# Kernel optimization log

Measured on AMD Instinct MI355X. Metric: run time of the kernel, lower is better.

Reference implementation:

```python
import jax, jax.numpy as jnp
import numpy as np

E = 256  # embed_dim (hardcoded in source module)
H = 4    # n_head
D = E // H
SEQ = 32768


def setup_inputs() -> dict:
    key = jax.random.key(0)
    ks = jax.random.split(key, 5)
    x = jax.random.normal(ks[0], (SEQ, E), dtype=jnp.float32)
    in_proj_weight = jax.random.normal(ks[1], (3 * E, E), dtype=jnp.float32) * (1.0 / np.sqrt(E))
    in_proj_bias = jax.random.normal(ks[2], (3 * E,), dtype=jnp.float32) * 0.02
    out_proj_weight = jax.random.normal(ks[3], (E, E), dtype=jnp.float32) * (1.0 / np.sqrt(E))
    out_proj_bias = jax.random.normal(ks[4], (E,), dtype=jnp.float32) * 0.02
    return {
        "x": x,
        "in_proj_weight": in_proj_weight,
        "in_proj_bias": in_proj_bias,
        "out_proj_weight": out_proj_weight,
        "out_proj_bias": out_proj_bias,
    }


def reference(x, in_proj_weight, in_proj_bias, out_proj_weight, out_proj_bias):
    # QKV projections (q uses only the first token of x: single-query decode attention)
    Wq, Wk, Wv = in_proj_weight[:E], in_proj_weight[E:2 * E], in_proj_weight[2 * E:]
    bq, bk, bv = in_proj_bias[:E], in_proj_bias[E:2 * E], in_proj_bias[2 * E:]
    q = x[:1] @ Wq.T + bq            # [1, E]
    k = x @ Wk.T + bk                # [S, E]
    v = x @ Wv.T + bv                # [S, E]

    qh = q.reshape(H, D)             # [H, D] (single query)
    kh = k.reshape(-1, H, D)         # [S, H, D]
    vh = v.reshape(-1, H, D)         # [S, H, D]

    scale = 1.0 / np.sqrt(D).astype(np.float32)
    scores = jnp.einsum("hd,shd->hs", qh, kh) * scale   # [H, S]
    attn = jax.nn.softmax(scores, axis=-1)                # [H, S]
    ctx = jnp.einsum("hs,shd->hd", attn, vh)             # [H, D]

    out = ctx.reshape(1, E) @ out_proj_weight.T + out_proj_bias  # [1, E]
    return out
```

## Files before the change

### kernel.cpp

```cpp
#include <hip/hip_runtime.h>

#define S 32768
#define NBLK 256
#define WS_C4   0
#define WS_KQ   64
#define WS_MP   1088
#define WS_LP   2112
#define WS_YV   3136
#define WS_B2   4160
#define WS_M2   4416
#define WS_YP   266560
#define WS_CNT  528704

__device__ __forceinline__ float dot4(float4 a, float4 b) {
  return a.x * b.x + a.y * b.y + a.z * b.z + a.w * b.w;
}

__device__ __forceinline__ void signal_done(int* p) {
  __threadfence();
  __syncthreads();
  if (threadIdx.x == 0) atomicAdd(p, 1);
}
__device__ __forceinline__ void spin_until(int* p, int target) {
  if (threadIdx.x == 0) {
    while (atomicAdd(p, 0) < target) __builtin_amdgcn_s_sleep(2);
  }
  __syncthreads();
  __threadfence();
}
__device__ __forceinline__ int take_ticket(int* p, int* shi) {
  __threadfence();
  __syncthreads();
  if (threadIdx.x == 0) *shi = atomicAdd(p, 1);
  __syncthreads();
  return *shi;
}

__device__ __forceinline__ void phaseA_kq(const float* __restrict__ x, const float* __restrict__ W,
                                          const float* __restrict__ inb, float* __restrict__ kq,
                                          float* __restrict__ c4, float* sh, int bid, int t) {
  float* xs = sh;
  float* qls = sh + 256;
  float* red = sh + 320;
  const int lane = t & 63, w = t >> 6;
  const int h = bid >> 2, qt = bid & 3;
  if (t < 256) xs[t] = x[t];
  __syncthreads();
  const float4 xv = *(const float4*)&xs[lane * 4];
#pragma unroll
  for (int k = 0; k < 8; ++k) {
    const int eloc = w * 8 + k;
    const int row = h * 64 + eloc;
    float4 wv = *(const float4*)&W[(size_t)row * 256 + lane * 4];
    float p = dot4(wv, xv);
#pragma unroll
    for (int m = 1; m < 64; m <<= 1) p += __shfl_xor(p, m);
    if (lane == 0) qls[eloc] = p + inb[row];
  }
  __syncthreads();
  const int cl = t & 63, ds = t >> 6;
  float acc = 0.f;
#pragma unroll
  for (int d2 = 0; d2 < 8; ++d2) {
    const int d = ds * 8 + d2;
    acc += W[(size_t)(256 + h * 64 + d) * 256 + qt * 64 + cl] * qls[d];
  }
  red[ds * 64 + cl] = acc;
  __syncthreads();
  if (ds == 0) {
    float s = 0.f;
#pragma unroll
    for (int i = 0; i < 8; ++i) s += red[i * 64 + cl];
    kq[h * 256 + qt * 64 + cl] = s;
  }
  if (qt == 0 && t < 64) {
    float v = qls[t] * inb[256 + h * 64 + t];
#pragma unroll
    for (int m = 1; m < 64; m <<= 1) v += __shfl_xor(v, m);
    if (t == 0) c4[h] = v;
  }
}

__device__ __forceinline__ void phaseA_m2(const float* __restrict__ W, const float* __restrict__ Wout,
                                          float* __restrict__ M2, float* sh, int b2, int t) {
  float* wout_t = sh;
  const int tile = b2 >> 1, sub = b2 & 1;
  const int h = tile >> 4, e0 = (tile & 15) * 16 + sub * 8;
  {
    const int e = t >> 6, d = t & 63;
    wout_t[e * 64 + d] = Wout[(size_t)(e0 + e) * 256 + h * 64 + d];
  }
  __syncthreads();
  const int c = t & 255, eh = t >> 8;
  float acc[4] = {0.f, 0.f, 0.f, 0.f};
#pragma unroll 8
  for (int d = 0; d < 64; ++d) {
    const float wv = W[(size_t)(512 + h * 64 + d) * 256 + c];
#pragma unroll
    for (int e = 0; e < 4; ++e) acc[e] += wv * wout_t[(eh * 4 + e) * 64 + d];
  }
#pragma unroll
  for (int e = 0; e < 4; ++e)
    M2[(size_t)(e0 + eh * 4 + e) * 1024 + h * 256 + c] = acc[e];
}

__device__ __forceinline__ void phaseA_b2(const float* __restrict__ Wout, const float* __restrict__ inb,
                                          const float* __restrict__ bout, float* __restrict__ bias2,
                                          float* sh, int b, int t) {
  float* red = sh;
  const int og = t >> 5, seg = t & 31;
  const int e = b * 16 + og;
  float acc = 0.f;
#pragma unroll
  for (int j = 0; j < 8; ++j)
    acc += Wout[(size_t)e * 256 + seg * 8 + j] * inb[512 + seg * 8 + j];
  red[og * 32 + seg] = acc;
  __syncthreads();
  if (t < 16) {
    float s = bout[b * 16 + t];
#pragma unroll
    for (int i = 0; i < 32; ++i) s += red[t * 32 + i];
    bias2[b * 16 + t] = s;
  }
}

__device__ __forceinline__ float bscore(float4 xv, float4 kq0, float4 kq1, float4 kq2,
                                        float4 kq3, float c4v, int lane) {
  float p0 = dot4(xv, kq0), p1 = dot4(xv, kq1), p2 = dot4(xv, kq2), p3 = dot4(xv, kq3);
  const bool b1 = (lane & 2) != 0;
  float keep0 = b1 ? p2 : p0, send0 = b1 ? p0 : p2;
  keep0 += __shfl_xor(send0, 2);
  float keep1 = b1 ? p3 : p1, send1 = b1 ? p1 : p3;
  keep1 += __shfl_xor(send1, 2);
  const bool b0 = (lane & 1) != 0;
  float vv = b0 ? keep1 : keep0, sv = b0 ? keep0 : keep1;
  vv += __shfl_xor(sv, 1);
  vv += __shfl_xor(vv, 4);
  vv += __shfl_xor(vv, 8);
  vv += __shfl_xor(vv, 16);
  vv += __shfl_xor(vv, 32);
  return (vv + c4v) * 0.125f;
}

__device__ __forceinline__ void phaseB_core(const float4* xvA, const float4* xvB,
                                            const float* __restrict__ kq, const float* __restrict__ c4,
                                            float* __restrict__ ypart, float* __restrict__ mpart,
                                            float* __restrict__ lpart, float* sh, int bid, int t) {
  float* yls = sh;
  float* sml = sh + 8192;
  float* sll = sh + 8224;
  const int lane = t & 63, w = t >> 6;
  const int hme = lane & 3;
  const float4 kq0 = *(const float4*)&kq[0 * 256 + lane * 4];
  const float4 kq1 = *(const float4*)&kq[1 * 256 + lane * 4];
  const float4 kq2 = *(const float4*)&kq[2 * 256 + lane * 4];
  const float4 kq3 = *(const float4*)&kq[3 * 256 + lane * 4];
  const float c4v = c4[hme];

  float vA[8];
#pragma unroll
  for (int r = 0; r < 8; ++r) vA[r] = bscore(xvA[r], kq0, kq1, kq2, kq3, c4v, lane);
  float m = vA[0];
#pragma unroll
  for (int r = 1; r < 8; ++r) m = fmaxf(m, vA[r]);

  float l = 0.f;
  float4 a[4];
#pragma unroll
  for (int k = 0; k < 4; ++k) a[k] = (float4){0.f, 0.f, 0.f, 0.f};
#pragma unroll
  for (int r = 0; r < 8; ++r) {
    const float e0 = __expf(vA[r] - m);
    l += e0;
    const float e1 = __shfl_xor(e0, 1);
    const float e2 = __shfl_xor(e0, 2);
    const float e3 = __shfl_xor(e0, 3);
    a[0].x += e0 * xvA[r].x; a[0].y += e0 * xvA[r].y; a[0].z += e0 * xvA[r].z; a[0].w += e0 * xvA[r].w;
    a[1].x += e1 * xvA[r].x; a[1].y += e1 * xvA[r].y; a[1].z += e1 * xvA[r].z; a[1].w += e1 * xvA[r].w;
    a[2].x += e2 * xvA[r].x; a[2].y += e2 * xvA[r].y; a[2].z += e2 * xvA[r].z; a[2].w += e2 * xvA[r].w;
    a[3].x += e3 * xvA[r].x; a[3].y += e3 * xvA[r].y; a[3].z += e3 * xvA[r].z; a[3].w += e3 * xvA[r].w;
  }

  float vB[8];
#pragma unroll
  for (int r = 0; r < 8; ++r) vB[r] = bscore(xvB[r], kq0, kq1, kq2, kq3, c4v, lane);
  float mB = vB[0];
#pragma unroll
  for (int r = 1; r < 8; ++r) mB = fmaxf(mB, vB[r]);

  {
    const float mN = fmaxf(m, mB);
    const float fown = __expf(m - mN);
    l *= fown;
    const float f1 = __shfl_xor(fown, 1);
    const float f2 = __shfl_xor(fown, 2);
    const float f3 = __shfl_xor(fown, 3);
    a[0].x *= fown; a[0].y *= fown; a[0].z *= fown; a[0].w *= fown;
    a[1].x *= f1;   a[1].y *= f1;   a[1].z *= f1;   a[1].w *= f1;
    a[2].x *= f2;   a[2].y *= f2;   a[2].z *= f2;   a[2].w *= f2;
    a[3].x *= f3;   a[3].y *= f3;   a[3].z *= f3;   a[3].w *= f3;
    m = mN;
  }
#pragma unroll
  for (int r = 0; r < 8; ++r) {
    const float e0 = __expf(vB[r] - m);
    l += e0;
    const float e1 = __shfl_xor(e0, 1);
    const float e2 = __shfl_xor(e0, 2);
    const float e3 = __shfl_xor(e0, 3);
    a[0].x += e0 * xvB[r].x; a[0].y += e0 * xvB[r].y; a[0].z += e0 * xvB[r].z; a[0].w += e0 * xvB[r].w;
    a[1].x += e1 * xvB[r].x; a[1].y += e1 * xvB[r].y; a[1].z += e1 * xvB[r].z; a[1].w += e1 * xvB[r].w;
    a[2].x += e2 * xvB[r].x; a[2].y += e2 * xvB[r].y; a[2].z += e2 * xvB[r].z; a[2].w += e2 * xvB[r].w;
    a[3].x += e3 * xvB[r].x; a[3].y += e3 * xvB[r].y; a[3].z += e3 * xvB[r].z; a[3].w += e3 * xvB[r].w;
  }

  __syncthreads();
  if (lane < 4) { sml[w * 4 + lane] = m; sll[w * 4 + lane] = l; }
  __syncthreads();

#pragma unroll
  for (int k = 0; k < 4; ++k) {
    const int h = hme ^ k;
    float mb = sml[h];
#pragma unroll
    for (int i = 1; i < 8; ++i) mb = fmaxf(mb, sml[i * 4 + h]);
    const float f = __expf(sml[w * 4 + h] - mb);
    float4 av;
    av.x = a[k].x * f; av.y = a[k].y * f; av.z = a[k].z * f; av.w = a[k].w * f;
    *(float4*)&yls[w * 1024 + h * 256 + lane * 4] = av;
  }
  __syncthreads();

  if (t < 4) {
    float mb = sml[t];
#pragma unroll
    for (int i = 1; i < 8; ++i) mb = fmaxf(mb, sml[i * 4 + t]);
    float lb = 0.f;
#pragma unroll
    for (int i = 0; i < 8; ++i) lb += sll[i * 4 + t] * __expf(sml[i * 4 + t] - mb);
    mpart[t * NBLK + bid] = mb;
    lpart[t * NBLK + bid] = lb;
  }
  float* yp = &ypart[(size_t)bid * 1024];
#pragma unroll
  for (int o = t; o < 1024; o += 512) {
    float s = 0.f;
#pragma unroll
    for (int i = 0; i < 8; ++i) s += yls[i * 1024 + o];
    yp[o] = s;
  }
}

__device__ __forceinline__ void phaseC(const float* __restrict__ ypart, const float* __restrict__ mpart,
                                       const float* __restrict__ lpart, float* __restrict__ yv,
                                       float* sh, int bid, int t) {
  float* mred = sh;
  float* scales = sh + 256;
  float* lred = sh + 512;
  float* sred = sh + 768;
  const int h = bid >> 4;
  const int o0 = bid * 16;
  if (t < 256) mred[t] = mpart[h * 256 + t];
  __syncthreads();
  for (int s = 128; s > 0; s >>= 1) {
    if (t < s) mred[t] = fmaxf(mred[t], mred[t + s]);
    __syncthreads();
  }
  const float mg = mred[0];
  if (t < 256) {
    const float sc = __expf(mpart[h * 256 + t] - mg);
    scales[t] = sc;
    lred[t] = lpart[h * 256 + t] * sc;
  }
  __syncthreads();
  for (int s = 128; s > 0; s >>= 1) {
    if (t < s) lred[t] += lred[t + s];
    __syncthreads();
  }
  const float inv = 1.0f / lred[0];
  const int ol = t & 15, bg = t >> 4;
  float s = 0.f;
#pragma unroll
  for (int j = 0; j < 8; ++j) {
    const int b = bg * 8 + j;
    s += ypart[(size_t)b * 1024 + o0 + ol] * scales[b];
  }
  sred[bg * 16 + ol] = s;
  __syncthreads();
  if (t < 16) {
    float tot = 0.f;
#pragma unroll
    for (int g = 0; g < 32; ++g) tot += sred[g * 16 + t];
    yv[o0 + t] = tot * inv;
  }
}

__device__ __forceinline__ void phaseD(const float* __restrict__ M2, const float* __restrict__ yv,
                                       const float* __restrict__ bias2, float* __restrict__ out,
                                       float* sh, int bid, int t) {
  float* yls = sh;
  float* smo = sh + 1024;
  for (int i = t; i < 1024; i += 512) yls[i] = yv[i];
  __syncthreads();
  const int og = t >> 5, seg = t & 31;
  const int e = bid * 16 + og;
  float acc = 0.f;
  const float4* m4 = (const float4*)&M2[(size_t)e * 1024 + seg * 32];
  const float4* y4 = (const float4*)&yls[seg * 32];
#pragma unroll
  for (int j = 0; j < 8; ++j) acc += dot4(m4[j], y4[j]);
  smo[og * 32 + seg] = acc;
  __syncthreads();
  if (t < 16) {
    float s = bias2[bid * 16 + t];
#pragma unroll
    for (int i = 0; i < 32; ++i) s += smo[t * 32 + i];
    out[bid * 16 + t] = s;
  }
}

__global__ void __launch_bounds__(512, 1) mha_coop(const float* __restrict__ x,
                                                   const float* __restrict__ W,
                                                   const float* __restrict__ inb,
                                                   const float* __restrict__ Wout,
                                                   const float* __restrict__ bout,
                                                   float* __restrict__ out,
                                                   float* __restrict__ ws) {
  __shared__ __align__(16) float sh[8448];
  __shared__ int shi;
  const int t = threadIdx.x, bid = blockIdx.x;
  const int lane = t & 63, w = t >> 6;
  int* cnt = (int*)(ws + WS_CNT);
  float* c4 = ws + WS_C4;
  float* kq = ws + WS_KQ;
  float* mpart = ws + WS_MP;
  float* lpart = ws + WS_LP;
  float* yv = ws + WS_YV;
  float* bias2 = ws + WS_B2;
  float* M2 = ws + WS_M2;
  float* ypart = ws + WS_YP;

  const int r0 = bid * 128 + w * 16;
  float4 xvA[8], xvB[8];

  if (bid >= 16) {
#pragma unroll
    for (int r = 0; r < 8; ++r)
      xvA[r] = *(const float4*)&x[(size_t)(r0 + r) * 256 + lane * 4];
#pragma unroll
    for (int r = 0; r < 8; ++r)
      xvB[r] = *(const float4*)&x[(size_t)(r0 + 8 + r) * 256 + lane * 4];
  }

  if (bid < 16) {
    phaseA_kq(x, W, inb, kq, c4, sh, bid, t);
    signal_done(&cnt[0]);
#pragma unroll
    for (int r = 0; r < 8; ++r)
      xvA[r] = *(const float4*)&x[(size_t)(r0 + r) * 256 + lane * 4];
#pragma unroll
    for (int r = 0; r < 8; ++r)
      xvB[r] = *(const float4*)&x[(size_t)(r0 + 8 + r) * 256 + lane * 4];
  } else if (bid < 144) {
    phaseA_m2(W, Wout, M2, sh, bid - 16, t);
    signal_done(&cnt[1]);
  } else if (bid < 160) {
    phaseA_b2(Wout, inb, bout, bias2, sh, bid - 144, t);
    signal_done(&cnt[1]);
  }

  spin_until(&cnt[0], 16);
  phaseB_core(xvA, xvB, kq, c4, ypart, mpart, lpart, sh, bid, t);

  const int tk = take_ticket(&cnt[2], &shi);
  if (tk < NBLK - 64) return;
  spin_until(&cnt[2], NBLK);
  phaseC(ypart, mpart, lpart, yv, sh, tk - (NBLK - 64), t);

  const int t2 = take_ticket(&cnt[3], &shi);
  if (t2 < 48) return;
  spin_until(&cnt[3], 64);
  spin_until(&cnt[1], 144);
  phaseD(M2, yv, bias2, out, sh, t2 - 48, t);
}

__global__ void __launch_bounds__(512) fb_A(const float* __restrict__ x, const float* __restrict__ W,
                                            const float* __restrict__ inb, const float* __restrict__ Wout,
                                            const float* __restrict__ bout, float* __restrict__ ws) {
  __shared__ __align__(16) float sh[832];
  const int bid = blockIdx.x, t = threadIdx.x;
  if (bid < 16) phaseA_kq(x, W, inb, ws + WS_KQ, ws + WS_C4, sh, bid, t);
  else if (bid < 144) phaseA_m2(W, Wout, ws + WS_M2, sh, bid - 16, t);
  else if (bid < 160) phaseA_b2(Wout, inb, bout, ws + WS_B2, sh, bid - 144, t);
}
__global__ void __launch_bounds__(512) fb_B(const float* __restrict__ x, float* __restrict__ ws) {
  __shared__ __align__(16) float sh[8256];
  const int bid = blockIdx.x, t = threadIdx.x;
  const int lane = t & 63, w = t >> 6;
  const int r0 = bid * 128 + w * 16;
  float4 xvA[8], xvB[8];
#pragma unroll
  for (int r = 0; r < 8; ++r)
    xvA[r] = *(const float4*)&x[(size_t)(r0 + r) * 256 + lane * 4];
#pragma unroll
  for (int r = 0; r < 8; ++r)
    xvB[r] = *(const float4*)&x[(size_t)(r0 + 8 + r) * 256 + lane * 4];
  phaseB_core(xvA, xvB, ws + WS_KQ, ws + WS_C4, ws + WS_YP, ws + WS_MP, ws + WS_LP, sh, bid, t);
}
__global__ void __launch_bounds__(512) fb_C(float* __restrict__ ws) {
  __shared__ __align__(16) float sh[1280];
  phaseC(ws + WS_YP, ws + WS_MP, ws + WS_LP, ws + WS_YV, sh, blockIdx.x, threadIdx.x);
}
__global__ void __launch_bounds__(512) fb_D(float* __restrict__ out, float* __restrict__ ws) {
  __shared__ __align__(16) float sh[1536];
  phaseD(ws + WS_M2, ws + WS_YV, ws + WS_B2, out, sh, blockIdx.x, threadIdx.x);
}

extern "C" void kernel_launch(void* const* d_in, const int* in_sizes, int n_in,
                              void* d_out, int out_size, void* d_ws, size_t ws_size,
                              hipStream_t stream) {
  const float* x = (const float*)d_in[0];
  const float* W = (const float*)d_in[1];
  const float* inb = (const float*)d_in[2];
  const float* Wout = (const float*)d_in[3];
  const float* bout = (const float*)d_in[4];
  float* out = (float*)d_out;
  float* ws = (float*)d_ws;

  hipMemsetAsync((void*)(ws + WS_CNT), 0, 16, stream);

  int dev = 0;
  (void)hipGetDevice(&dev);
  int coopAttr = 0, ncu = 0, occ = 0;
  bool coop = (hipDeviceGetAttribute(&coopAttr, hipDeviceAttributeCooperativeLaunch, dev) == hipSuccess) &&
              coopAttr != 0;
  coop = coop &&
         (hipDeviceGetAttribute(&ncu, hipDeviceAttributeMultiprocessorCount, dev) == hipSuccess);
  coop = coop &&
         (hipOccupancyMaxActiveBlocksPerMultiprocessor(&occ, mha_coop, 512, 0) == hipSuccess);
  coop = coop && (occ * ncu >= NBLK);

  if (coop) {
    void* args[] = {(void*)&x, (void*)&W, (void*)&inb, (void*)&Wout,
                    (void*)&bout, (void*)&out, (void*)&ws};
    if (hipLaunchCooperativeKernel((const void*)mha_coop, dim3(NBLK), dim3(512),
                                   args, 0, stream) == hipSuccess)
      return;
  }
  fb_A<<<160, 512, 0, stream>>>(x, W, inb, Wout, bout, ws);
  fb_B<<<NBLK, 512, 0, stream>>>(x, ws);
  fb_C<<<64, 512, 0, stream>>>(ws);
  fb_D<<<16, 512, 0, stream>>>(out, ws);
}
```

Before: 36.03 us.

## Compute kq redundantly per block and replace ticket spins with grid sync

Every block now computes the full Wk^T q vector and per-head bias constants in shared memory, so the start of the score phase no longer waits on a global counter. The M2 and bias2 precomputation moves to run after the score phase in the upper blocks. Inter-phase coordination uses a cooperative-groups grid.sync followed by a single acquire counter before the final projection, which is split across 64 blocks instead of 16. This trades redundant weight reads in every block for fewer global synchronization points and a shorter critical path.

```diff
diff --git a/kernel.cpp b/kernel.cpp
--- a/kernel.cpp
+++ b/kernel.cpp
@@ -1,84 +1,88 @@
 #include <hip/hip_runtime.h>
-
-#define S 32768
+#include <hip/hip_cooperative_groups.h>
+namespace cg = cooperative_groups;
+
 #define NBLK 256
-#define WS_C4   0
-#define WS_KQ   64
-#define WS_MP   1088
-#define WS_LP   2112
-#define WS_YV   3136
-#define WS_B2   4160
-#define WS_M2   4416
-#define WS_YP   266560
-#define WS_CNT  528704
+#define WS_MP   0
+#define WS_LP   1024
+#define WS_YV   2048
+#define WS_B2   3072
+#define WS_M2   3328
+#define WS_YP   265472
+#define WS_CNT  527616
 
 __device__ __forceinline__ float dot4(float4 a, float4 b) {
   return a.x * b.x + a.y * b.y + a.z * b.z + a.w * b.w;
 }
 
-__device__ __forceinline__ void signal_done(int* p) {
+__device__ __forceinline__ void sig_rel(int* p) {
   __threadfence();
   __syncthreads();
   if (threadIdx.x == 0) atomicAdd(p, 1);
 }
-__device__ __forceinline__ void spin_until(int* p, int target) {
+__device__ __forceinline__ void spin_acq(int* p, int target) {
   if (threadIdx.x == 0) {
-    while (atomicAdd(p, 0) < target) __builtin_amdgcn_s_sleep(2);
+    while (__hip_atomic_load(p, __ATOMIC_ACQUIRE, __HIP_MEMORY_SCOPE_AGENT) < target)
+      __builtin_amdgcn_s_sleep(8);
   }
   __syncthreads();
   __threadfence();
 }
-__device__ __forceinline__ int take_ticket(int* p, int* shi) {
-  __threadfence();
-  __syncthreads();
-  if (threadIdx.x == 0) *shi = atomicAdd(p, 1);
-  __syncthreads();
-  return *shi;
-}
-
-__device__ __forceinline__ void phaseA_kq(const float* __restrict__ x, const float* __restrict__ W,
-                                          const float* __restrict__ inb, float* __restrict__ kq,
-                                          float* __restrict__ c4, float* sh, int bid, int t) {
-  float* xs = sh;
-  float* qls = sh + 256;
-  float* red = sh + 320;
+
+__device__ __forceinline__ void make_kq(const float* __restrict__ x, const float* __restrict__ W,
+                                        const float* __restrict__ inb,
+                                        float* xs, float* qls, float* kqls, float* c4ls,
+                                        float* red2, int t) {
   const int lane = t & 63, w = t >> 6;
-  const int h = bid >> 2, qt = bid & 3;
   if (t < 256) xs[t] = x[t];
   __syncthreads();
-  const float4 xv = *(const float4*)&xs[lane * 4];
-#pragma unroll
-  for (int k = 0; k < 8; ++k) {
-    const int eloc = w * 8 + k;
-    const int row = h * 64 + eloc;
-    float4 wv = *(const float4*)&W[(size_t)row * 256 + lane * 4];
-    float p = dot4(wv, xv);
-#pragma unroll
-    for (int m = 1; m < 64; m <<= 1) p += __shfl_xor(p, m);
-    if (lane == 0) qls[eloc] = p + inb[row];
-  }
-  __syncthreads();
-  const int cl = t & 63, ds = t >> 6;
-  float acc = 0.f;
-#pragma unroll
-  for (int d2 = 0; d2 < 8; ++d2) {
-    const int d = ds * 8 + d2;
-    acc += W[(size_t)(256 + h * 64 + d) * 256 + qt * 64 + cl] * qls[d];
-  }
-  red[ds * 64 + cl] = acc;
-  __syncthreads();
-  if (ds == 0) {
-    float s = 0.f;
-#pragma unroll
-    for (int i = 0; i < 8; ++i) s += red[i * 64 + cl];
-    kq[h * 256 + qt * 64 + cl] = s;
-  }
-  if (qt == 0 && t < 64) {
-    float v = qls[t] * inb[256 + h * 64 + t];
+  const float4 xv0 = *(const float4*)&xs[lane * 4];
+  for (int k = 0; k < 32; k += 4) {
+    float p[4];
+#pragma unroll
+    for (int j = 0; j < 4; ++j) {
+      const int row = w * 32 + k + j;
+      float4 wv = *(const float4*)&W[(size_t)row * 256 + lane * 4];
+      p[j] = dot4(wv, xv0);
+    }
+#pragma unroll
+    for (int m = 1; m < 64; m <<= 1) {
+#pragma unroll
+      for (int j = 0; j < 4; ++j) p[j] += __shfl_xor(p[j], m);
+    }
+    if (lane == 0) {
+#pragma unroll
+      for (int j = 0; j < 4; ++j) qls[w * 32 + k + j] = p[j] + inb[w * 32 + k + j];
+    }
+  }
+  __syncthreads();
+  const int c = t & 255, g = t >> 8;
+  float acc0 = 0.f, acc1 = 0.f, acc2 = 0.f, acc3 = 0.f;
+#pragma unroll 4
+  for (int dd = 0; dd < 32; ++dd) {
+    const int d = g * 32 + dd;
+    acc0 += W[(size_t)(256 + 0 * 64 + d) * 256 + c] * qls[0 * 64 + d];
+    acc1 += W[(size_t)(256 + 1 * 64 + d) * 256 + c] * qls[1 * 64 + d];
+    acc2 += W[(size_t)(256 + 2 * 64 + d) * 256 + c] * qls[2 * 64 + d];
+    acc3 += W[(size_t)(256 + 3 * 64 + d) * 256 + c] * qls[3 * 64 + d];
+  }
+  red2[g * 1024 + 0 * 256 + c] = acc0;
+  red2[g * 1024 + 1 * 256 + c] = acc1;
+  red2[g * 1024 + 2 * 256 + c] = acc2;
+  red2[g * 1024 + 3 * 256 + c] = acc3;
+  __syncthreads();
+  if (g == 0) {
+#pragma unroll
+    for (int h = 0; h < 4; ++h)
+      kqls[h * 256 + c] = red2[h * 256 + c] + red2[1024 + h * 256 + c];
+  } else {
+    const int hh = w - 4;
+    float v = qls[hh * 64 + lane] * inb[256 + hh * 64 + lane];
 #pragma unroll
     for (int m = 1; m < 64; m <<= 1) v += __shfl_xor(v, m);
-    if (t == 0) c4[h] = v;
-  }
+    if (lane == 0) c4ls[hh] = v;
+  }
+  __syncthreads();
 }
 
 __device__ __forceinline__ void phaseA_m2(const float* __restrict__ W, const float* __restrict__ Wout,
@@ -143,12 +147,11 @@
 }
 
 __device__ __forceinline__ void phaseB_core(const float4* xvA, const float4* xvB,
-                                            const float* __restrict__ kq, const float* __restrict__ c4,
+                                            const float* kq, const float* c4,
                                             float* __restrict__ ypart, float* __restrict__ mpart,
-                                            float* __restrict__ lpart, float* sh, int bid, int t) {
-  float* yls = sh;
-  float* sml = sh + 8192;
-  float* sll = sh + 8224;
+                                            float* __restrict__ lpart, float* yls, int bid, int t) {
+  float* sml = yls + 8192;
+  float* sll = yls + 8224;
   const int lane = t & 63, w = t >> 6;
   const int hme = lane & 3;
   const float4 kq0 = *(const float4*)&kq[0 * 256 + lane * 4];
@@ -295,107 +298,42 @@
   }
 }
 
-__device__ __forceinline__ void phaseD(const float* __restrict__ M2, const float* __restrict__ yv,
-                                       const float* __restrict__ bias2, float* __restrict__ out,
-                                       float* sh, int bid, int t) {
-  float* yls = sh;
+__device__ __forceinline__ void phaseD4(const float* __restrict__ M2, const float* __restrict__ yv,
+                                        const float* __restrict__ bias2, float* __restrict__ out,
+                                        float* sh, int bid, int t) {
+  float* yls2 = sh;
   float* smo = sh + 1024;
-  for (int i = t; i < 1024; i += 512) yls[i] = yv[i];
-  __syncthreads();
-  const int og = t >> 5, seg = t & 31;
-  const int e = bid * 16 + og;
-  float acc = 0.f;
-  const float4* m4 = (const float4*)&M2[(size_t)e * 1024 + seg * 32];
-  const float4* y4 = (const float4*)&yls[seg * 32];
-#pragma unroll
-  for (int j = 0; j < 8; ++j) acc += dot4(m4[j], y4[j]);
-  smo[og * 32 + seg] = acc;
-  __syncthreads();
-  if (t < 16) {
-    float s = bias2[bid * 16 + t];
-#pragma unroll
-    for (int i = 0; i < 32; ++i) s += smo[t * 32 + i];
-    out[bid * 16 + t] = s;
-  }
-}
-
-__global__ void __launch_bounds__(512, 1) mha_coop(const float* __restrict__ x,
-                                                   const float* __restrict__ W,
-                                                   const float* __restrict__ inb,
-                                                   const float* __restrict__ Wout,
-                                                   const float* __restrict__ bout,
-                                                   float* __restrict__ out,
-                                                   float* __restrict__ ws) {
-  __shared__ __align__(16) float sh[8448];
-  __shared__ int shi;
-  const int t = threadIdx.x, bid = blockIdx.x;
   const int lane = t & 63, w = t >> 6;
-  int* cnt = (int*)(ws + WS_CNT);
-  float* c4 = ws + WS_C4;
-  float* kq = ws + WS_KQ;
-  float* mpart = ws + WS_MP;
-  float* lpart = ws + WS_LP;
-  float* yv = ws + WS_YV;
+  for (int i = t; i < 1024; i += 512) yls2[i] = yv[i];
+  __syncthreads();
+  const int eidx = t >> 7, seg = t & 127;
+  const int e = bid * 4 + eidx;
+  const float4* m4 = (const float4*)&M2[(size_t)e * 1024];
+  const float4* y4 = (const float4*)yls2;
+  float acc = dot4(m4[seg * 2], y4[seg * 2]) + dot4(m4[seg * 2 + 1], y4[seg * 2 + 1]);
+#pragma unroll
+  for (int m = 1; m < 64; m <<= 1) acc += __shfl_xor(acc, m);
+  if (lane == 0) smo[w] = acc;
+  __syncthreads();
+  if (t < 4) out[bid * 4 + t] = smo[2 * t] + smo[2 * t + 1] + bias2[bid * 4 + t];
+}
+
+__device__ __forceinline__ void phase1(const float* __restrict__ x, const float* __restrict__ W,
+                                       const float* __restrict__ inb, const float* __restrict__ Wout,
+                                       const float* __restrict__ bout, float* sh, float* ws,
+                                       int bid, int t) {
   float* bias2 = ws + WS_B2;
   float* M2 = ws + WS_M2;
   float* ypart = ws + WS_YP;
-
-  const int r0 = bid * 128 + w * 16;
-  float4 xvA[8], xvB[8];
-
-  if (bid >= 16) {
-#pragma unroll
-    for (int r = 0; r < 8; ++r)
-      xvA[r] = *(const float4*)&x[(size_t)(r0 + r) * 256 + lane * 4];
-#pragma unroll
-    for (int r = 0; r < 8; ++r)
-      xvB[r] = *(const float4*)&x[(size_t)(r0 + 8 + r) * 256 + lane * 4];
-  }
-
-  if (bid < 16) {
-    phaseA_kq(x, W, inb, kq, c4, sh, bid, t);
-    signal_done(&cnt[0]);
-#pragma unroll
-    for (int r = 0; r < 8; ++r)
-      xvA[r] = *(const float4*)&x[(size_t)(r0 + r) * 256 + lane * 4];
-#pragma unroll
-    for (int r = 0; r < 8; ++r)
-      xvB[r] = *(const float4*)&x[(size_t)(r0 + 8 + r) * 256 + lane * 4];
-  } else if (bid < 144) {
-    phaseA_m2(W, Wout, M2, sh, bid - 16, t);
-    signal_done(&cnt[1]);
-  } else if (bid < 160) {
-    phaseA_b2(Wout, inb, bout, bias2, sh, bid - 144, t);
-    signal_done(&cnt[1]);
-  }
-
-  spin_until(&cnt[0], 16);
-  phaseB_core(xvA, xvB, kq, c4, ypart, mpart, lpart, sh, bid, t);
-
-  const int tk = take_ticket(&cnt[2], &shi);
-  if (tk < NBLK - 64) return;
-  spin_until(&cnt[2], NBLK);
-  phaseC(ypart, mpart, lpart, yv, sh, tk - (NBLK - 64), t);
-
-  const int t2 = take_ticket(&cnt[3], &shi);
-  if (t2 < 48) return;
-  spin_until(&cnt[3], 64);
-  spin_until(&cnt[1], 144);
-  phaseD(M2, yv, bias2, out, sh, t2 - 48, t);
-}
-
-__global__ void __launch_bounds__(512) fb_A(const float* __restrict__ x, const float* __restrict__ W,
-                                            const float* __restrict__ inb, const float* __restrict__ Wout,
-                                            const float* __restrict__ bout, float* __restrict__ ws) {
-  __shared__ __align__(16) float sh[832];
-  const int bid = blockIdx.x, t = threadIdx.x;
-  if (bid < 16) phaseA_kq(x, W, inb, ws + WS_KQ, ws + WS_C4, sh, bid, t);
-  else if (bid < 144) phaseA_m2(W, Wout, ws + WS_M2, sh, bid - 16, t);
-  else if (bid < 160) phaseA_b2(Wout, inb, bout, ws + WS_B2, sh, bid - 144, t);
-}
-__global__ void __launch_bounds__(512) fb_B(const float* __restrict__ x, float* __restrict__ ws) {
-  __shared__ __align__(16) float sh[8256];
-  const int bid = blockIdx.x, t = threadIdx.x;
+  float* mpart = ws + WS_MP;
+  float* lpart = ws + WS_LP;
+  float* xs = sh;
+  float* qls = sh + 256;
+  float* kqls = sh + 512;
+  float* c4ls = sh + 1536;
+  float* red2 = sh + 1540;
+  float* yls = sh + 1540;
+
   const int lane = t & 63, w = t >> 6;
   const int r0 = bid * 128 + w * 16;
   float4 xvA[8], xvB[8];
@@ -405,15 +343,52 @@
 #pragma unroll
   for (int r = 0; r < 8; ++r)
     xvB[r] = *(const float4*)&x[(size_t)(r0 + 8 + r) * 256 + lane * 4];
-  phaseB_core(xvA, xvB, ws + WS_KQ, ws + WS_C4, ws + WS_YP, ws + WS_MP, ws + WS_LP, sh, bid, t);
-}
-__global__ void __launch_bounds__(512) fb_C(float* __restrict__ ws) {
+
+  make_kq(x, W, inb, xs, qls, kqls, c4ls, red2, t);
+  phaseB_core(xvA, xvB, kqls, c4ls, ypart, mpart, lpart, yls, bid, t);
+
+  if (bid >= 128) {
+    phaseA_m2(W, Wout, M2, sh, bid - 128, t);
+    if (bid >= 240) {
+      __syncthreads();
+      phaseA_b2(Wout, inb, bout, bias2, sh, bid - 240, t);
+    }
+  }
+}
+
+__global__ void __launch_bounds__(512, 1) mha_one(const float* __restrict__ x,
+                                                  const float* __restrict__ W,
+                                                  const float* __restrict__ inb,
+                                                  const float* __restrict__ Wout,
+                                                  const float* __restrict__ bout,
+                                                  float* __restrict__ out,
+                                                  float* __restrict__ ws) {
+  __shared__ __align__(16) float sh[9796];
+  const int t = threadIdx.x, bid = blockIdx.x;
+  cg::grid_group grid = cg::this_grid();
+
+  phase1(x, W, inb, Wout, bout, sh, ws, bid, t);
+  grid.sync();
+  if (bid >= 64) return;
+  phaseC(ws + WS_YP, ws + WS_MP, ws + WS_LP, ws + WS_YV, sh, bid, t);
+  sig_rel((int*)(ws + WS_CNT));
+  spin_acq((int*)(ws + WS_CNT), 64);
+  phaseD4(ws + WS_M2, ws + WS_YV, ws + WS_B2, out, sh, bid, t);
+}
+
+__global__ void __launch_bounds__(512) fb_1(const float* __restrict__ x, const float* __restrict__ W,
+                                            const float* __restrict__ inb, const float* __restrict__ Wout,
+                                            const float* __restrict__ bout, float* __restrict__ ws) {
+  __shared__ __align__(16) float sh[9796];
+  phase1(x, W, inb, Wout, bout, sh, ws, blockIdx.x, threadIdx.x);
+}
+__global__ void __launch_bounds__(512) fb_2(float* __restrict__ ws) {
   __shared__ __align__(16) float sh[1280];
   phaseC(ws + WS_YP, ws + WS_MP, ws + WS_LP, ws + WS_YV, sh, blockIdx.x, threadIdx.x);
 }
-__global__ void __launch_bounds__(512) fb_D(float* __restrict__ out, float* __restrict__ ws) {
-  __shared__ __align__(16) float sh[1536];
-  phaseD(ws + WS_M2, ws + WS_YV, ws + WS_B2, out, sh, blockIdx.x, threadIdx.x);
+__global__ void __launch_bounds__(512) fb_3(float* __restrict__ out, float* __restrict__ ws) {
+  __shared__ __align__(16) float sh[1056];
+  phaseD4(ws + WS_M2, ws + WS_YV, ws + WS_B2, out, sh, blockIdx.x, threadIdx.x);
 }
 
 extern "C" void kernel_launch(void* const* d_in, const int* in_sizes, int n_in,
@@ -437,18 +412,17 @@
   coop = coop &&
          (hipDeviceGetAttribute(&ncu, hipDeviceAttributeMultiprocessorCount, dev) == hipSuccess);
   coop = coop &&
-         (hipOccupancyMaxActiveBlocksPerMultiprocessor(&occ, mha_coop, 512, 0) == hipSuccess);
+         (hipOccupancyMaxActiveBlocksPerMultiprocessor(&occ, mha_one, 512, 0) == hipSuccess);
   coop = coop && (occ * ncu >= NBLK);
 
   if (coop) {
     void* args[] = {(void*)&x, (void*)&W, (void*)&inb, (void*)&Wout,
                     (void*)&bout, (void*)&out, (void*)&ws};
-    if (hipLaunchCooperativeKernel((const void*)mha_coop, dim3(NBLK), dim3(512),
+    if (hipLaunchCooperativeKernel((const void*)mha_one, dim3(NBLK), dim3(512),
                                    args, 0, stream) == hipSuccess)
       return;
   }
-  fb_A<<<160, 512, 0, stream>>>(x, W, inb, Wout, bout, ws);
-  fb_B<<<NBLK, 512, 0, stream>>>(x, ws);
-  fb_C<<<64, 512, 0, stream>>>(ws);
-  fb_D<<<16, 512, 0, stream>>>(out, ws);
-}
+  fb_1<<<NBLK, 512, 0, stream>>>(x, W, inb, Wout, bout, ws);
+  fb_2<<<64, 512, 0, stream>>>(ws);
+  fb_3<<<64, 512, 0, stream>>>(out, ws);
+}
```

Result: slower. 54.58 us (+51.5%).

## Replace counter barriers with per-block flags and move M2 work after scores

Applied to the files above, without the earlier changes.

Swaps the shared atomic counters and ticket scheme for per-block release/acquire flags that whole blocks poll with syncthreads_and. The M2/bias2 precomputation moves off the critical path: instead of running before phase B on blocks 16-159, it runs after phase B on blocks 128-255, so phase B can start sooner. Phase D is spread over 64 blocks with wave-shuffle reductions, and the flag memset grows to 2 KB. The cost is more polling traffic, and M2 may now finish late and stall phase D.

```diff
diff --git a/kernel.cpp b/kernel.cpp
--- a/kernel.cpp
+++ b/kernel.cpp
@@ -1,13 +1,12 @@
 #include <hip/hip_runtime.h>
 
-#define S 32768
 #define NBLK 256
-#define WS_C4   0
-#define WS_KQ   64
-#define WS_MP   1088
-#define WS_LP   2112
-#define WS_YV   3136
-#define WS_B2   4160
+#define WS_MP   0
+#define WS_LP   1024
+#define WS_YV   2048
+#define WS_B2   3072
+#define WS_KQ   3328
+#define WS_C4   4352
 #define WS_M2   4416
 #define WS_YP   266560
 #define WS_CNT  528704
@@ -16,24 +15,19 @@
   return a.x * b.x + a.y * b.y + a.z * b.z + a.w * b.w;
 }
 
-__device__ __forceinline__ void signal_done(int* p) {
+__device__ __forceinline__ void set_flag(int* slot, int t) {
   __threadfence();
   __syncthreads();
-  if (threadIdx.x == 0) atomicAdd(p, 1);
-}
-__device__ __forceinline__ void spin_until(int* p, int target) {
-  if (threadIdx.x == 0) {
-    while (atomicAdd(p, 0) < target) __builtin_amdgcn_s_sleep(2);
-  }
-  __syncthreads();
+  if (t == 0) __hip_atomic_store(slot, 1, __ATOMIC_RELEASE, __HIP_MEMORY_SCOPE_AGENT);
+}
+__device__ __forceinline__ void poll_flags(const int* flags, int n, int t) {
+  const int idx = t & (n - 1);
+  for (;;) {
+    int v = __hip_atomic_load((int*)&flags[idx], __ATOMIC_RELAXED, __HIP_MEMORY_SCOPE_AGENT);
+    if (__syncthreads_and(v != 0)) break;
+    __builtin_amdgcn_s_sleep(2);
+  }
   __threadfence();
-}
-__device__ __forceinline__ int take_ticket(int* p, int* shi) {
-  __threadfence();
-  __syncthreads();
-  if (threadIdx.x == 0) *shi = atomicAdd(p, 1);
-  __syncthreads();
-  return *shi;
 }
 
 __device__ __forceinline__ void phaseA_kq(const float* __restrict__ x, const float* __restrict__ W,
@@ -81,8 +75,10 @@
   }
 }
 
-__device__ __forceinline__ void phaseA_m2(const float* __restrict__ W, const float* __restrict__ Wout,
-                                          float* __restrict__ M2, float* sh, int b2, int t) {
+__device__ __forceinline__ void phaseM2b(const float* __restrict__ W, const float* __restrict__ Wout,
+                                         const float* __restrict__ inb, const float* __restrict__ bout,
+                                         float* __restrict__ M2, float* __restrict__ bias2,
+                                         float* sh, int b2, int t) {
   float* wout_t = sh;
   const int tile = b2 >> 1, sub = b2 & 1;
   const int h = tile >> 4, e0 = (tile & 15) * 16 + sub * 8;
@@ -102,26 +98,17 @@
 #pragma unroll
   for (int e = 0; e < 4; ++e)
     M2[(size_t)(e0 + eh * 4 + e) * 1024 + h * 256 + c] = acc[e];
-}
-
-__device__ __forceinline__ void phaseA_b2(const float* __restrict__ Wout, const float* __restrict__ inb,
-                                          const float* __restrict__ bout, float* __restrict__ bias2,
-                                          float* sh, int b, int t) {
+  __syncthreads();
   float* red = sh;
-  const int og = t >> 5, seg = t & 31;
-  const int e = b * 16 + og;
-  float acc = 0.f;
-#pragma unroll
-  for (int j = 0; j < 8; ++j)
-    acc += Wout[(size_t)e * 256 + seg * 8 + j] * inb[512 + seg * 8 + j];
-  red[og * 32 + seg] = acc;
-  __syncthreads();
-  if (t < 16) {
-    float s = bout[b * 16 + t];
-#pragma unroll
-    for (int i = 0; i < 32; ++i) s += red[t * 32 + i];
-    bias2[b * 16 + t] = s;
-  }
+  const int oi = t >> 8, seg = t & 255;
+  const int e = 2 * b2 + oi;
+  red[oi * 256 + seg] = Wout[(size_t)e * 256 + seg] * inb[512 + seg];
+  __syncthreads();
+  for (int s = 128; s > 0; s >>= 1) {
+    if (seg < s) red[oi * 256 + seg] += red[oi * 256 + seg + s];
+    __syncthreads();
+  }
+  if (t < 2) bias2[2 * b2 + t] = red[t * 256] + bout[2 * b2 + t];
 }
 
 __device__ __forceinline__ float bscore(float4 xv, float4 kq0, float4 kq1, float4 kq2,
@@ -145,10 +132,9 @@
 __device__ __forceinline__ void phaseB_core(const float4* xvA, const float4* xvB,
                                             const float* __restrict__ kq, const float* __restrict__ c4,
                                             float* __restrict__ ypart, float* __restrict__ mpart,
-                                            float* __restrict__ lpart, float* sh, int bid, int t) {
-  float* yls = sh;
-  float* sml = sh + 8192;
-  float* sll = sh + 8224;
+                                            float* __restrict__ lpart, float* yls, int bid, int t) {
+  float* sml = yls + 8192;
+  float* sll = yls + 8224;
   const int lane = t & 63, w = t >> 6;
   const int hme = lane & 3;
   const float4 kq0 = *(const float4*)&kq[0 * 256 + lane * 4];
@@ -295,50 +281,40 @@
   }
 }
 
-__device__ __forceinline__ void phaseD(const float* __restrict__ M2, const float* __restrict__ yv,
-                                       const float* __restrict__ bias2, float* __restrict__ out,
-                                       float* sh, int bid, int t) {
-  float* yls = sh;
+__device__ __forceinline__ void phaseD4(const float* __restrict__ M2, const float* __restrict__ yv,
+                                        const float* __restrict__ bias2, float* __restrict__ out,
+                                        float* sh, int bid, int t) {
+  float* yls2 = sh;
   float* smo = sh + 1024;
-  for (int i = t; i < 1024; i += 512) yls[i] = yv[i];
-  __syncthreads();
-  const int og = t >> 5, seg = t & 31;
-  const int e = bid * 16 + og;
-  float acc = 0.f;
-  const float4* m4 = (const float4*)&M2[(size_t)e * 1024 + seg * 32];
-  const float4* y4 = (const float4*)&yls[seg * 32];
-#pragma unroll
-  for (int j = 0; j < 8; ++j) acc += dot4(m4[j], y4[j]);
-  smo[og * 32 + seg] = acc;
-  __syncthreads();
-  if (t < 16) {
-    float s = bias2[bid * 16 + t];
-#pragma unroll
-    for (int i = 0; i < 32; ++i) s += smo[t * 32 + i];
-    out[bid * 16 + t] = s;
-  }
-}
-
-__global__ void __launch_bounds__(512, 1) mha_coop(const float* __restrict__ x,
-                                                   const float* __restrict__ W,
-                                                   const float* __restrict__ inb,
-                                                   const float* __restrict__ Wout,
-                                                   const float* __restrict__ bout,
-                                                   float* __restrict__ out,
-                                                   float* __restrict__ ws) {
-  __shared__ __align__(16) float sh[8448];
-  __shared__ int shi;
+  const int lane = t & 63, w = t >> 6;
+  for (int i = t; i < 1024; i += 512) yls2[i] = yv[i];
+  __syncthreads();
+  const int seg = t & 127;
+  const int e = bid * 4 + (t >> 7);
+  const float4* m4 = (const float4*)&M2[(size_t)e * 1024];
+  const float4* y4 = (const float4*)yls2;
+  float acc = dot4(m4[seg * 2], y4[seg * 2]) + dot4(m4[seg * 2 + 1], y4[seg * 2 + 1]);
+#pragma unroll
+  for (int m = 1; m < 64; m <<= 1) acc += __shfl_xor(acc, m);
+  if (lane == 0) smo[w] = acc;
+  __syncthreads();
+  if (t < 4) out[bid * 4 + t] = smo[2 * t] + smo[2 * t + 1] + bias2[bid * 4 + t];
+}
+
+__global__ void __launch_bounds__(512, 1) mha_one(const float* __restrict__ x,
+                                                  const float* __restrict__ W,
+                                                  const float* __restrict__ inb,
+                                                  const float* __restrict__ Wout,
+                                                  const float* __restrict__ bout,
+                                                  float* __restrict__ out,
+                                                  float* __restrict__ ws) {
+  __shared__ __align__(16) float sh[8256];
   const int t = threadIdx.x, bid = blockIdx.x;
   const int lane = t & 63, w = t >> 6;
-  int* cnt = (int*)(ws + WS_CNT);
-  float* c4 = ws + WS_C4;
-  float* kq = ws + WS_KQ;
-  float* mpart = ws + WS_MP;
-  float* lpart = ws + WS_LP;
-  float* yv = ws + WS_YV;
-  float* bias2 = ws + WS_B2;
-  float* M2 = ws + WS_M2;
-  float* ypart = ws + WS_YP;
+  int* flagA = (int*)(ws + WS_CNT);
+  int* flagB = flagA + 16;
+  int* flagC = flagB + 256;
+  int* flagM = flagC + 64;
 
   const int r0 = bid * 128 + w * 16;
   float4 xvA[8], xvB[8];
@@ -350,48 +326,40 @@
 #pragma unroll
     for (int r = 0; r < 8; ++r)
       xvB[r] = *(const float4*)&x[(size_t)(r0 + 8 + r) * 256 + lane * 4];
-  }
-
-  if (bid < 16) {
-    phaseA_kq(x, W, inb, kq, c4, sh, bid, t);
-    signal_done(&cnt[0]);
+  } else {
+    phaseA_kq(x, W, inb, ws + WS_KQ, ws + WS_C4, sh, bid, t);
+    set_flag(&flagA[bid], t);
 #pragma unroll
     for (int r = 0; r < 8; ++r)
       xvA[r] = *(const float4*)&x[(size_t)(r0 + r) * 256 + lane * 4];
 #pragma unroll
     for (int r = 0; r < 8; ++r)
       xvB[r] = *(const float4*)&x[(size_t)(r0 + 8 + r) * 256 + lane * 4];
-  } else if (bid < 144) {
-    phaseA_m2(W, Wout, M2, sh, bid - 16, t);
-    signal_done(&cnt[1]);
-  } else if (bid < 160) {
-    phaseA_b2(Wout, inb, bout, bias2, sh, bid - 144, t);
-    signal_done(&cnt[1]);
-  }
-
-  spin_until(&cnt[0], 16);
-  phaseB_core(xvA, xvB, kq, c4, ypart, mpart, lpart, sh, bid, t);
-
-  const int tk = take_ticket(&cnt[2], &shi);
-  if (tk < NBLK - 64) return;
-  spin_until(&cnt[2], NBLK);
-  phaseC(ypart, mpart, lpart, yv, sh, tk - (NBLK - 64), t);
-
-  const int t2 = take_ticket(&cnt[3], &shi);
-  if (t2 < 48) return;
-  spin_until(&cnt[3], 64);
-  spin_until(&cnt[1], 144);
-  phaseD(M2, yv, bias2, out, sh, t2 - 48, t);
+  }
+
+  poll_flags(flagA, 16, t);
+  phaseB_core(xvA, xvB, ws + WS_KQ, ws + WS_C4, ws + WS_YP, ws + WS_MP, ws + WS_LP, sh, bid, t);
+  set_flag(&flagB[bid], t);
+
+  if (bid >= 128) {
+    phaseM2b(W, Wout, inb, bout, ws + WS_M2, ws + WS_B2, sh, bid - 128, t);
+    set_flag(&flagM[bid - 128], t);
+    return;
+  }
+  if (bid >= 64) return;
+
+  poll_flags(flagB, 256, t);
+  phaseC(ws + WS_YP, ws + WS_MP, ws + WS_LP, ws + WS_YV, sh, bid, t);
+  set_flag(&flagC[bid], t);
+  poll_flags(flagC, 64, t);
+  poll_flags(flagM, 128, t);
+  phaseD4(ws + WS_M2, ws + WS_YV, ws + WS_B2, out, sh, bid, t);
 }
 
 __global__ void __launch_bounds__(512) fb_A(const float* __restrict__ x, const float* __restrict__ W,
-                                            const float* __restrict__ inb, const float* __restrict__ Wout,
-                                            const float* __restrict__ bout, float* __restrict__ ws) {
+                                            const float* __restrict__ inb, float* __restrict__ ws) {
   __shared__ __align__(16) float sh[832];
-  const int bid = blockIdx.x, t = threadIdx.x;
-  if (bid < 16) phaseA_kq(x, W, inb, ws + WS_KQ, ws + WS_C4, sh, bid, t);
-  else if (bid < 144) phaseA_m2(W, Wout, ws + WS_M2, sh, bid - 16, t);
-  else if (bid < 160) phaseA_b2(Wout, inb, bout, ws + WS_B2, sh, bid - 144, t);
+  phaseA_kq(x, W, inb, ws + WS_KQ, ws + WS_C4, sh, blockIdx.x, threadIdx.x);
 }
 __global__ void __launch_bounds__(512) fb_B(const float* __restrict__ x, float* __restrict__ ws) {
   __shared__ __align__(16) float sh[8256];
@@ -407,13 +375,17 @@
     xvB[r] = *(const float4*)&x[(size_t)(r0 + 8 + r) * 256 + lane * 4];
   phaseB_core(xvA, xvB, ws + WS_KQ, ws + WS_C4, ws + WS_YP, ws + WS_MP, ws + WS_LP, sh, bid, t);
 }
-__global__ void __launch_bounds__(512) fb_C(float* __restrict__ ws) {
+__global__ void __launch_bounds__(512) fb_CM(const float* __restrict__ W, const float* __restrict__ Wout,
+                                             const float* __restrict__ inb, const float* __restrict__ bout,
+                                             float* __restrict__ ws) {
   __shared__ __align__(16) float sh[1280];
-  phaseC(ws + WS_YP, ws + WS_MP, ws + WS_LP, ws + WS_YV, sh, blockIdx.x, threadIdx.x);
+  const int bid = blockIdx.x, t = threadIdx.x;
+  if (bid < 64) phaseC(ws + WS_YP, ws + WS_MP, ws + WS_LP, ws + WS_YV, sh, bid, t);
+  else phaseM2b(W, Wout, inb, bout, ws + WS_M2, ws + WS_B2, sh, bid - 64, t);
 }
 __global__ void __launch_bounds__(512) fb_D(float* __restrict__ out, float* __restrict__ ws) {
-  __shared__ __align__(16) float sh[1536];
-  phaseD(ws + WS_M2, ws + WS_YV, ws + WS_B2, out, sh, blockIdx.x, threadIdx.x);
+  __shared__ __align__(16) float sh[1056];
+  phaseD4(ws + WS_M2, ws + WS_YV, ws + WS_B2, out, sh, blockIdx.x, threadIdx.x);
 }
 
 extern "C" void kernel_launch(void* const* d_in, const int* in_sizes, int n_in,
@@ -427,7 +399,7 @@
   float* out = (float*)d_out;
   float* ws = (float*)d_ws;
 
-  hipMemsetAsync((void*)(ws + WS_CNT), 0, 16, stream);
+  hipMemsetAsync((void*)(ws + WS_CNT), 0, 2048, stream);
 
   int dev = 0;
   (void)hipGetDevice(&dev);
@@ -437,18 +409,18 @@
   coop = coop &&
          (hipDeviceGetAttribute(&ncu, hipDeviceAttributeMultiprocessorCount, dev) == hipSuccess);
   coop = coop &&
-         (hipOccupancyMaxActiveBlocksPerMultiprocessor(&occ, mha_coop, 512, 0) == hipSuccess);
+         (hipOccupancyMaxActiveBlocksPerMultiprocessor(&occ, mha_one, 512, 0) == hipSuccess);
   coop = coop && (occ * ncu >= NBLK);
 
   if (coop) {
     void* args[] = {(void*)&x, (void*)&W, (void*)&inb, (void*)&Wout,
                     (void*)&bout, (void*)&out, (void*)&ws};
-    if (hipLaunchCooperativeKernel((const void*)mha_coop, dim3(NBLK), dim3(512),
+    if (hipLaunchCooperativeKernel((const void*)mha_one, dim3(NBLK), dim3(512),
                                    args, 0, stream) == hipSuccess)
       return;
   }
-  fb_A<<<160, 512, 0, stream>>>(x, W, inb, Wout, bout, ws);
+  fb_A<<<16, 512, 0, stream>>>(x, W, inb, ws);
   fb_B<<<NBLK, 512, 0, stream>>>(x, ws);
-  fb_C<<<64, 512, 0, stream>>>(ws);
-  fb_D<<<16, 512, 0, stream>>>(out, ws);
-}
+  fb_CM<<<192, 512, 0, stream>>>(W, Wout, inb, bout, ws);
+  fb_D<<<64, 512, 0, stream>>>(out, ws);
+}
```

Result: no change. 36.05 us (+0.0%).
